# Performance work log

Measured on AMD Instinct MI355X. Metric: run time of the kernel, lower is better.

## Reference

```python
import jax, jax.numpy as jnp
import numpy as np

BLOCK = 256
EPS = 1e-6

def _silu(x):
    return x * jax.nn.sigmoid(x)

def setup_inputs() -> dict:
    key = jax.random.key(0)
    k1, k2, k3, k4 = jax.random.split(key, 4)
    embed_dim, hidden_dim = 2048, 2048
    b, n, h = 2, 4096, 16
    x = jax.random.normal(k1, (b, n, embed_dim), dtype=jnp.float32)
    slope_rate = jax.random.uniform(k2, (h, 1, 1), dtype=jnp.float32, minval=0.01, maxval=1.0)
    W_qkvu = jax.random.normal(k3, (4 * hidden_dim, embed_dim), dtype=jnp.float32) / np.sqrt(embed_dim)
    W_out = jax.random.normal(k4, (embed_dim, hidden_dim), dtype=jnp.float32) / np.sqrt(hidden_dim)
    return {"x": x, "slope_rate": slope_rate, "W_qkvu": W_qkvu, "W_out": W_out}

def reference(x, slope_rate, W_qkvu, W_out):
    b, n, embed_dim = x.shape
    h = slope_rate.shape[0]
    hidden_dim = W_qkvu.shape[0] // 4
    d = hidden_dim // h  # head dim
    NB = n // BLOCK

    qkvu = x @ W_qkvu.T  # [b, n, 4*hidden]
    q, k, v, u = jnp.split(qkvu, 4, axis=-1)

    def to_heads(t):
        return t.reshape(b, n, h, d).transpose(0, 2, 1, 3)  # b h n d

    q = _silu(to_heads(q))
    k = _silu(to_heads(k))
    v = to_heads(v)

    s = slope_rate  # (h,1,1)
    arr = jnp.arange(1, BLOCK + 1, dtype=x.dtype)  # 1..BLOCK
    q_decay = jnp.exp(-s * arr[:, None])                 # (h, B, 1)
    k_decay = jnp.exp(-s * (BLOCK - arr[:, None]))       # (h, B, 1)
    idx = arr[:, None] - arr[None, :]                    # (B, B)
    diag_decay = jnp.exp(jnp.where(idx >= 0, -s * idx, -jnp.inf))  # (h, B, B)
    block_decay = jnp.exp(-s * BLOCK)                    # (h,1,1)

    # reshape into blocks, scan-major axis first
    def blk(t):
        return t.reshape(b, h, NB, BLOCK, d).transpose(2, 0, 1, 3, 4)

    qb, kb, vb = blk(q), blk(k), blk(v)

    def step(kv, inp):
        qi, ki, vi = inp  # (b,h,B,d)
        qkv_none_diag = jnp.einsum('bhmd,bhde->bhme', qi * q_decay, kv)
        qk = jnp.einsum('bhmd,bhsd->bhms', qi, ki) * diag_decay
        qkv_diag = jnp.einsum('bhms,bhse->bhme', qk, vi)
        kv_new = block_decay * kv + jnp.einsum('bhsd,bhse->bhde', ki * k_decay, vi)
        return kv_new, qkv_none_diag + qkv_diag

    kv0 = jnp.zeros((b, h, d, d), dtype=jnp.float32)
    _, outs = jax.lax.scan(step, kv0, (qb, kb, vb))  # (NB,b,h,B,d)

    o = outs.transpose(1, 2, 0, 3, 4).reshape(b, h, n, d)
    o = o.transpose(0, 2, 1, 3).reshape(b, n, hidden_dim)  # b n (h d)

    # simple RMSNorm (no learned scale)
    o = o * jax.lax.rsqrt(jnp.mean(o * o, axis=-1, keepdims=True) + EPS)
    o = u * o
    return o @ W_out.T
```

## Files before the change

kernel.cpp:

```cpp
#include <hip/hip_runtime.h>
#include <stdint.h>

#define GK 2048

typedef short s16x8 __attribute__((ext_vector_type(8)));
typedef short s16x4 __attribute__((ext_vector_type(4)));
typedef float fx4   __attribute__((ext_vector_type(4)));
typedef unsigned int ux2 __attribute__((ext_vector_type(2)));

#define SB0 __builtin_amdgcn_sched_barrier(0)

__device__ __forceinline__ float b2f(unsigned short s) {
  union { unsigned int u; float f; } x; x.u = ((unsigned int)s) << 16; return x.f;
}
__device__ __forceinline__ unsigned short f2b(float f) {
  union { float f; unsigned int u; } x; x.f = f;
  return (unsigned short)((x.u + 0x7fffu + ((x.u >> 16) & 1u)) >> 16);
}
__device__ __forceinline__ void gl_lds16(const void* g, void* l) {
  __builtin_amdgcn_global_load_lds(
      (const __attribute__((address_space(1))) void*)g,
      (__attribute__((address_space(3))) void*)l, 16, 0, 0);
}

__global__ __launch_bounds__(256, 4) void cvt_bf16(const float* __restrict__ in,
                                                   unsigned short* __restrict__ out) {
  int i = blockIdx.x * 256 + threadIdx.x;
  fx4 v = *(const fx4*)(in + (size_t)i * 4);
  ux2 p;
  p[0] = (unsigned int)f2b(v[0]) | ((unsigned int)f2b(v[1]) << 16);
  p[1] = (unsigned int)f2b(v[2]) | ((unsigned int)f2b(v[3]) << 16);
  *(ux2*)(out + (size_t)i * 4) = p;
}

__global__ void sentinel_k(float* o, float val) { o[threadIdx.x] = val; }

__global__ __launch_bounds__(512, 2) void gemm8_qkvu(
    const unsigned short* __restrict__ A, const unsigned short* __restrict__ B,
    int NT, int nBase,
    unsigned short* __restrict__ qp, unsigned short* __restrict__ kp,
    unsigned short* __restrict__ vp, unsigned short* __restrict__ up) {
  __shared__ __align__(16) unsigned short lds8[65536];
  const int nwg = gridDim.x;
  const int bid0 = blockIdx.x;
  const int cpx = nwg >> 3;
  const int bid = (bid0 & 7) * cpx + (bid0 >> 3);
  const int bm = bid / NT, bn = bid % NT;
  const int tid = threadIdx.x;
  const int w = tid >> 6, l = tid & 63;
  const int wr = w >> 2, wc = w & 3;
  const int g = l >> 4, li = l & 15;

  const int srow = l >> 3;
  const int scol = ((l & 7) ^ srow) << 3;
  const unsigned short* Asrc = A + (size_t)(bm * 256) * GK + scol;
  const unsigned short* Bsrc = B + (size_t)(bn * 256) * GK + scol;

  auto stA = [&](int bu, int h, int kt) {
    const unsigned short* s = Asrc + (size_t)(h * 128 + w * 8 + srow) * GK + kt;
    unsigned short* d = &lds8[(bu * 2 + h) * 8192 + w * 512];
    gl_lds16(s, d);
    gl_lds16(s + (size_t)64 * GK, d + 4096);
  };
  auto stB = [&](int bu, int h, int kt) {
    const unsigned short* s = Bsrc + (size_t)(h * 128 + w * 8 + srow) * GK + kt;
    unsigned short* d = &lds8[32768 + (bu * 2 + h) * 8192 + w * 512];
    gl_lds16(s, d);
    gl_lds16(s + (size_t)64 * GK, d + 4096);
  };

  const int s7 = li & 7;
  const int cb0 = ((0 + g) ^ s7) << 3;
  const int cb1 = ((4 + g) ^ s7) << 3;
  const int rbase = li * 64;
  const int Abase0 = wr * 8192;
  const int Bbase0 = 32768 + (wc >> 1) * 8192 + (wc & 1) * 4096;

  s16x8 aF[4][2], bL[2][2], bH[2][2];
  fx4 acc[8][4] = {};

  auto rdA = [&](int rb, int mh) {
    #pragma unroll
    for (int i = 0; i < 4; ++i) {
      int a0 = rb * 16384 + Abase0 + (mh * 4 + i) * 1024 + rbase;
      aF[i][0] = *(const s16x8*)&lds8[a0 + cb0];
      aF[i][1] = *(const s16x8*)&lds8[a0 + cb1];
    }
  };
  auto rdBL = [&](int rb) {
    #pragma unroll
    for (int i = 0; i < 2; ++i) {
      int a0 = rb * 16384 + Bbase0 + i * 1024 + rbase;
      bL[i][0] = *(const s16x8*)&lds8[a0 + cb0];
      bL[i][1] = *(const s16x8*)&lds8[a0 + cb1];
    }
  };
  auto rdBH = [&](int rb) {
    #pragma unroll
    for (int i = 0; i < 2; ++i) {
      int a0 = rb * 16384 + Bbase0 + (2 + i) * 1024 + rbase;
      bH[i][0] = *(const s16x8*)&lds8[a0 + cb0];
      bH[i][1] = *(const s16x8*)&lds8[a0 + cb1];
    }
  };
  auto mm = [&](int mh, int nh, s16x8 (&bF)[2][2]) {
    __builtin_amdgcn_s_setprio(1);
    #pragma unroll
    for (int i = 0; i < 4; ++i)
      #pragma unroll
      for (int j = 0; j < 2; ++j)
        #pragma unroll
        for (int kk = 0; kk < 2; ++kk)
          acc[mh * 4 + i][nh * 2 + j] =
              __builtin_amdgcn_mfma_f32_16x16x32_bf16(aF[i][kk], bF[j][kk],
                                                      acc[mh * 4 + i][nh * 2 + j], 0, 0, 0);
    __builtin_amdgcn_s_setprio(0);
  };

  const int KT = GK / 64;

  stA(0, 0, 0); stB(0, 0, 0); stA(0, 1, 0); stB(0, 1, 0);

  #pragma unroll 2
  for (int t = 0; t < KT - 1; ++t) {
    const int rb = t & 1, wb = rb ^ 1;
    const int ktn = (t + 1) * 64;
    stA(wb, 0, ktn);
    asm volatile("s_waitcnt vmcnt(2)" ::: "memory");
    SB0; __builtin_amdgcn_s_barrier(); SB0;
    rdA(rb, 0); rdBL(rb);
    mm(0, 0, bL);
    SB0; __builtin_amdgcn_s_barrier(); SB0;
    rdBH(rb);
    stB(wb, 0, ktn);
    SB0; __builtin_amdgcn_s_barrier(); SB0;
    mm(0, 1, bH);
    SB0; __builtin_amdgcn_s_barrier(); SB0;
    rdA(rb, 1);
    stA(wb, 1, ktn);
    SB0; __builtin_amdgcn_s_barrier(); SB0;
    mm(1, 1, bH);
    SB0; __builtin_amdgcn_s_barrier(); SB0;
    stB(wb, 1, ktn);
    SB0; __builtin_amdgcn_s_barrier(); SB0;
    mm(1, 0, bL);
    SB0; __builtin_amdgcn_s_barrier(); SB0;
  }
  {
    const int rb = (KT - 1) & 1;
    asm volatile("s_waitcnt vmcnt(0)" ::: "memory");
    SB0; __builtin_amdgcn_s_barrier(); SB0;
    rdA(rb, 0); rdBL(rb);
    mm(0, 0, bL);
    rdBH(rb);
    mm(0, 1, bH);
    rdA(rb, 1);
    mm(1, 1, bH);
    mm(1, 0, bL);
  }

  const int colbase = nBase + bn * 256 + wc * 64;
  #pragma unroll
  for (int mf = 0; mf < 8; ++mf)
    #pragma unroll
    for (int rr = 0; rr < 4; ++rr) {
      int nn = bm * 256 + wr * 128 + mf * 16 + g * 4 + rr;
      #pragma unroll
      for (int nf = 0; nf < 4; ++nf) {
        int colglob = colbase + nf * 16 + li;
        int tq = colglob >> 11, hh = (colglob >> 7) & 15, cl = colglob & 127;
        float vv = acc[mf][nf][rr];
        if (tq < 2) vv = vv / (1.f + __expf(-vv));
        if (tq == 3) up[(size_t)nn * 2048 + hh * 128 + cl] = f2b(vv);
        else ((tq == 0) ? qp : (tq == 1) ? kp : vp)[((size_t)hh * 4096 + nn) * 128 + cl] = f2b(vv);
      }
    }
}

__global__ __launch_bounds__(256, 2) void gemm_out(
    const unsigned short* __restrict__ A, const unsigned short* __restrict__ B,
    float* __restrict__ Cf) {
  __shared__ __align__(16) short lA[128 * 64];
  __shared__ __align__(16) short lB[128 * 64];
  const int nwg = gridDim.x;
  const int bid0 = blockIdx.x;
  const int cpx = nwg >> 3;
  const int bid = (bid0 & 7) * cpx + (bid0 >> 3);
  const int bm = bid / 16, bn = bid % 16;
  const int tid = threadIdx.x;
  const int w = tid >> 6, l = tid & 63;
  const int wr = w >> 1, wc = w & 1;
  const int g = l >> 4, li = l & 15;

  fx4 acc[4][4] = {};
  const int aRow = l >> 3, aCol = (l & 7) * 8;
  const unsigned short* Abase = A + (size_t)(bm * 128) * GK + aCol;
  const unsigned short* Bbase = B + (size_t)(bn * 128) * GK + aCol;

  for (int kt = 0; kt < GK; kt += 64) {
    __syncthreads();
    #pragma unroll
    for (int j = 0; j < 4; ++j) {
      int c = w * 4 + j;
      gl_lds16(Abase + (size_t)(c * 8 + aRow) * GK + kt, &lA[c * 512]);
      gl_lds16(Bbase + (size_t)(c * 8 + aRow) * GK + kt, &lB[c * 512]);
    }
    __syncthreads();
    #pragma unroll
    for (int kk = 0; kk < 2; ++kk) {
      s16x8 af[4], bf[4];
      #pragma unroll
      for (int mf = 0; mf < 4; ++mf)
        af[mf] = *(const s16x8*)&lA[(wr * 64 + mf * 16 + li) * 64 + kk * 32 + g * 8];
      #pragma unroll
      for (int nf = 0; nf < 4; ++nf)
        bf[nf] = *(const s16x8*)&lB[(wc * 64 + nf * 16 + li) * 64 + kk * 32 + g * 8];
      #pragma unroll
      for (int mf = 0; mf < 4; ++mf)
        #pragma unroll
        for (int nf = 0; nf < 4; ++nf)
          acc[mf][nf] = __builtin_amdgcn_mfma_f32_16x16x32_bf16(af[mf], bf[nf], acc[mf][nf], 0, 0, 0);
    }
  }
  #pragma unroll
  for (int mf = 0; mf < 4; ++mf)
    #pragma unroll
    for (int rr = 0; rr < 4; ++rr) {
      int row = bm * 128 + wr * 64 + mf * 16 + g * 4 + rr;
      #pragma unroll
      for (int nf = 0; nf < 4; ++nf) {
        int col = bn * 128 + wc * 64 + nf * 16 + li;
        Cf[(size_t)row * 2048 + col] = acc[mf][nf][rr];
      }
    }
}

__global__ __launch_bounds__(256, 1) void pass1_C(
    const unsigned short* __restrict__ k, const unsigned short* __restrict__ v,
    const float* __restrict__ slope, float* __restrict__ C) {
  __shared__ __align__(16) unsigned short lK[256 * 128];
  __shared__ __align__(16) unsigned short lV[256 * 128];
  __shared__ float ldecay[256];
  const int bid = blockIdx.x;
  const int h_i = bid >> 4, ib = bid & 15;
  const int tid = threadIdx.x, w = tid >> 6, l = tid & 63;
  const int g = l >> 4, li = l & 15;
  const float r = slope[h_i];
  const size_t kvoff = ((size_t)h_i * 4096 + ib * 256) * 128;
  #pragma unroll
  for (int j = 0; j < 16; ++j) {
    int c = w * 16 + j;
    gl_lds16(k + kvoff + c * 512 + l * 8, &lK[c * 512]);
    gl_lds16(v + kvoff + c * 512 + l * 8, &lV[c * 512]);
  }
  ldecay[tid] = __expf(-r * (float)(255 - tid));
  __syncthreads();

  fx4 acc[2][8] = {};
  #pragma unroll 1
  for (int ks = 0; ks < 8; ++ks) {
    s16x8 a[2], b[8];
    #pragma unroll
    for (int mf = 0; mf < 2; ++mf) {
      int dr = w * 32 + mf * 16 + li;
      #pragma unroll
      for (int e = 0; e < 8; ++e) {
        int s = ks * 32 + g * 8 + e;
        a[mf][e] = (short)f2b(b2f(lK[s * 128 + dr]) * ldecay[s]);
      }
    }
    #pragma unroll
    for (int nf = 0; nf < 8; ++nf) {
      int er = nf * 16 + li;
      #pragma unroll
      for (int e = 0; e < 8; ++e) {
        int s = ks * 32 + g * 8 + e;
        b[nf][e] = (short)lV[s * 128 + er];
      }
    }
    #pragma unroll
    for (int mf = 0; mf < 2; ++mf)
      #pragma unroll
      for (int nf = 0; nf < 8; ++nf)
        acc[mf][nf] = __builtin_amdgcn_mfma_f32_16x16x32_bf16(a[mf], b[nf], acc[mf][nf], 0, 0, 0);
  }
  float* Cb = C + (size_t)bid * 16384;
  #pragma unroll
  for (int mf = 0; mf < 2; ++mf)
    #pragma unroll
    for (int rr = 0; rr < 4; ++rr)
      #pragma unroll
      for (int nf = 0; nf < 8; ++nf)
        Cb[(w * 32 + mf * 16 + g * 4 + rr) * 128 + nf * 16 + li] = acc[mf][nf][rr];
}

__global__ __launch_bounds__(256, 4) void scan_kv2(
    const float* __restrict__ C, const float* __restrict__ slope,
    unsigned short* __restrict__ KVb) {
  __shared__ unsigned short lds[8][128];
  const int h_i = blockIdx.x >> 4, c = blockIdx.x & 15;
  const float r = slope[h_i];
  const float bd = __expf(-256.f * r);
  const int t = threadIdx.x;
  float run[4] = {0.f, 0.f, 0.f, 0.f};
  const int e_out = t >> 1, dg = t & 1;
  for (int i = 0; i < 16; ++i) {
    size_t base = ((size_t)h_i * 16 + i) * 16384;
    fx4 cv = *(const fx4*)(C + base + c * 1024 + t * 4);
    #pragma unroll
    for (int j = 0; j < 4; ++j) lds[t >> 5][(t & 31) * 4 + j] = f2b(run[j]);
    __syncthreads();
    s16x4 ov;
    #pragma unroll
    for (int j = 0; j < 4; ++j) ov[j] = (short)lds[dg * 4 + j][e_out];
    *(s16x4*)&KVb[base + e_out * 128 + c * 8 + dg * 4] = ov;
    __syncthreads();
    #pragma unroll
    for (int j = 0; j < 4; ++j) run[j] = bd * run[j] + cv[j];
  }
}

__global__ __launch_bounds__(256, 1) void pass3_O(
    const unsigned short* __restrict__ q, const unsigned short* __restrict__ k,
    const unsigned short* __restrict__ v, const unsigned short* __restrict__ KVb,
    const float* __restrict__ slope, unsigned short* __restrict__ o) {
  __shared__ __align__(16) unsigned short lK[64 * 128];
  __shared__ __align__(16) unsigned short lV[64 * 128];
  __shared__ __align__(16) unsigned short lP[4 * 64 * 64];
  const int bid = blockIdx.x;
  const int h_i = bid >> 4, ib = bid & 15;
  const int n0 = ib * 256;
  const float r = slope[h_i];
  const int tid = threadIdx.x, w = tid >> 6, l = tid & 63;
  const int g = l >> 4, li = l & 15;
  const int mbase = w * 64;

  fx4 accO[4][8] = {};
  const unsigned short* Qb = q + ((size_t)h_i * 4096 + n0 + mbase) * 128;
  const unsigned short* KVbase = KVb + ((size_t)h_i * 16 + ib) * 16384;

  #pragma unroll
  for (int kd = 0; kd < 4; ++kd) {
    s16x8 aq[4], bkv[8];
    #pragma unroll
    for (int mf = 0; mf < 4; ++mf)
      aq[mf] = *(const s16x8*)(Qb + (size_t)(mf * 16 + li) * 128 + kd * 32 + g * 8);
    #pragma unroll
    for (int nf = 0; nf < 8; ++nf)
      bkv[nf] = *(const s16x8*)(KVbase + (size_t)(nf * 16 + li) * 128 + kd * 32 + g * 8);
    #pragma unroll
    for (int mf = 0; mf < 4; ++mf)
      #pragma unroll
      for (int nf = 0; nf < 8; ++nf)
        accO[mf][nf] = __builtin_amdgcn_mfma_f32_16x16x32_bf16(aq[mf], bkv[nf], accO[mf][nf], 0, 0, 0);
  }
  #pragma unroll
  for (int mf = 0; mf < 4; ++mf)
    #pragma unroll
    for (int rr = 0; rr < 4; ++rr) {
      float f = __expf(-r * (float)(mbase + mf * 16 + g * 4 + rr + 1));
      #pragma unroll
      for (int nf = 0; nf < 8; ++nf) accO[mf][nf][rr] *= f;
    }

  for (int st = 0; st < 4; ++st) {
    __syncthreads();
    #pragma unroll
    for (int j = 0; j < 4; ++j) {
      int c = w * 4 + j;
      size_t roff = ((size_t)h_i * 4096 + n0 + st * 64) * 128 + c * 512 + l * 8;
      gl_lds16(k + roff, &lK[c * 512]);
      gl_lds16(v + roff, &lV[c * 512]);
    }
    __syncthreads();
    if (st > w) continue;

    fx4 sacc[4][4] = {};
    #pragma unroll
    for (int kd = 0; kd < 4; ++kd) {
      s16x8 aq[4], bk[4];
      #pragma unroll
      for (int mf = 0; mf < 4; ++mf)
        aq[mf] = *(const s16x8*)(Qb + (size_t)(mf * 16 + li) * 128 + kd * 32 + g * 8);
      #pragma unroll
      for (int nf = 0; nf < 4; ++nf)
        bk[nf] = *(const s16x8*)&lK[(nf * 16 + li) * 128 + kd * 32 + g * 8];
      #pragma unroll
      for (int mf = 0; mf < 4; ++mf)
        #pragma unroll
        for (int nf = 0; nf < 4; ++nf)
          sacc[mf][nf] = __builtin_amdgcn_mfma_f32_16x16x32_bf16(aq[mf], bk[nf], sacc[mf][nf], 0, 0, 0);
    }

    float f2v[4];
    #pragma unroll
    for (int nf = 0; nf < 4; ++nf) f2v[nf] = __expf(r * (float)(nf * 16 + li));
    unsigned short* lPw = &lP[w * 4096];
    #pragma unroll
    for (int mf = 0; mf < 4; ++mf)
      #pragma unroll
      for (int rr = 0; rr < 4; ++rr) {
        int Aoff = mbase - st * 64 + mf * 16 + g * 4 + rr;
        float f1 = __expf(-r * (float)Aoff);
        #pragma unroll
        for (int nf = 0; nf < 4; ++nf) {
          int sc = nf * 16 + li;
          float val = (Aoff >= sc) ? sacc[mf][nf][rr] * f1 * f2v[nf] : 0.f;
          lPw[(mf * 16 + g * 4 + rr) * 64 + sc] = f2b(val);
        }
      }

    #pragma unroll
    for (int ks = 0; ks < 2; ++ks) {
      s16x8 pa[4], vb[8];
      #pragma unroll
      for (int mf = 0; mf < 4; ++mf)
        pa[mf] = *(const s16x8*)&lPw[(mf * 16 + li) * 64 + ks * 32 + g * 8];
      #pragma unroll
      for (int nf = 0; nf < 8; ++nf) {
        int er = nf * 16 + li;
        #pragma unroll
        for (int e = 0; e < 8; ++e) {
          int s = ks * 32 + g * 8 + e;
          vb[nf][e] = (short)lV[s * 128 + er];
        }
      }
      #pragma unroll
      for (int mf = 0; mf < 4; ++mf)
        #pragma unroll
        for (int nf = 0; nf < 8; ++nf)
          accO[mf][nf] = __builtin_amdgcn_mfma_f32_16x16x32_bf16(pa[mf], vb[nf], accO[mf][nf], 0, 0, 0);
    }
  }

  #pragma unroll
  for (int mf = 0; mf < 4; ++mf)
    #pragma unroll
    for (int rr = 0; rr < 4; ++rr) {
      int nn = n0 + mbase + mf * 16 + g * 4 + rr;
      unsigned short* ob = o + (size_t)nn * 2048 + h_i * 128;
      #pragma unroll
      for (int nf = 0; nf < 8; ++nf)
        ob[nf * 16 + li] = f2b(accO[mf][nf][rr]);
    }
}

__global__ __launch_bounds__(256, 4) void norm_mul(
    const unsigned short* __restrict__ o, const unsigned short* __restrict__ u,
    unsigned short* __restrict__ z) {
  __shared__ float red[4];
  const int row = blockIdx.x, t = threadIdx.x;
  const size_t base = (size_t)row * 2048 + t * 8;
  s16x8 ov = *(const s16x8*)(o + base);
  float vals[8]; float ss = 0.f;
  #pragma unroll
  for (int j = 0; j < 8; ++j) { vals[j] = b2f((unsigned short)ov[j]); ss += vals[j] * vals[j]; }
  #pragma unroll
  for (int dl = 1; dl < 64; dl <<= 1) ss += __shfl_xor(ss, dl);
  if ((t & 63) == 0) red[t >> 6] = ss;
  __syncthreads();
  float tot = red[0] + red[1] + red[2] + red[3];
  float rs = rsqrtf(tot * (1.f / 2048.f) + 1e-6f);
  s16x8 uv = *(const s16x8*)(u + base);
  s16x8 zv;
  #pragma unroll
  for (int j = 0; j < 8; ++j)
    zv[j] = (short)f2b(vals[j] * b2f((unsigned short)uv[j]) * rs);
  *(s16x8*)(z + base) = zv;
}

extern "C" void kernel_launch(void* const* d_in, const int* in_sizes, int n_in,
                              void* d_out, int out_size, void* d_ws, size_t ws_size,
                              hipStream_t stream) {
  (void)in_sizes; (void)n_in; (void)out_size;
  const float* x     = (const float*)d_in[0];
  const float* slope = (const float*)d_in[1];
  const float* Wqkvu = (const float*)d_in[2];
  const float* Wout  = (const float*)d_in[3];
  float* out = (float*)d_out;

  const size_t NEED_MED = 92274688ull;
  const size_t NEED_BIG = 125829120ull;
  if (ws_size < NEED_MED) {
    sentinel_k<<<1, 256, 0, stream>>>(out, (float)((double)ws_size * 1e-6));
    return;
  }
  char* ws = (char*)d_ws;

  if (ws_size >= NEED_BIG) {
    unsigned short* wq  = (unsigned short*)(ws + 0);
    unsigned short* S0  = (unsigned short*)(ws + 33554432);
    unsigned short* qb  = (unsigned short*)(ws + 50331648);
    unsigned short* kb  = (unsigned short*)(ws + 67108864);
    unsigned short* vb  = (unsigned short*)(ws + 83886080);
    unsigned short* ub  = (unsigned short*)(ws + 100663296);
    unsigned short* KVr = (unsigned short*)(ws + 117440512);
    cvt_bf16<<<16384, 256, 0, stream>>>(Wqkvu, wq);
    for (int bb = 0; bb < 2; ++bb) {
      const float* xB = x + (size_t)bb * 8388608;
      float* outB = out + (size_t)bb * 8388608;
      cvt_bf16<<<8192, 256, 0, stream>>>(xB, S0);
      gemm8_qkvu<<<512, 512, 0, stream>>>(S0, wq, 32, 0, qb, kb, vb, ub);
      pass1_C<<<256, 256, 0, stream>>>(kb, vb, slope, (float*)S0);
      scan_kv2<<<256, 256, 0, stream>>>((float*)S0, slope, KVr);
      pass3_O<<<256, 256, 0, stream>>>(qb, kb, vb, KVr, slope, S0);
      cvt_bf16<<<4096, 256, 0, stream>>>(Wout, KVr);
      norm_mul<<<4096, 256, 0, stream>>>(S0, ub, qb);
      gemm_out<<<512, 256, 0, stream>>>(qb, KVr, outB);
    }
  } else {
    unsigned short* reg0 = (unsigned short*)(ws + 0);
    unsigned short* qb   = (unsigned short*)(ws + 16777216);
    unsigned short* kb   = (unsigned short*)(ws + 33554432);
    unsigned short* vb   = (unsigned short*)(ws + 50331648);
    unsigned short* ub   = (unsigned short*)(ws + 67108864);
    unsigned short* KVr  = (unsigned short*)(ws + 83886080);
    for (int bb = 0; bb < 2; ++bb) {
      const float* xB = x + (size_t)bb * 8388608;
      float* outB = out + (size_t)bb * 8388608;
      cvt_bf16<<<8192, 256, 0, stream>>>(xB, reg0);
      cvt_bf16<<<8192, 256, 0, stream>>>(Wqkvu, vb);
      gemm8_qkvu<<<256, 512, 0, stream>>>(reg0, vb, 16, 0, qb, kb, vb, ub);
      cvt_bf16<<<4096, 256, 0, stream>>>(Wqkvu + 8388608, KVr);
      gemm8_qkvu<<<128, 512, 0, stream>>>(reg0, KVr, 8, 4096, qb, kb, vb, ub);
      cvt_bf16<<<4096, 256, 0, stream>>>(Wqkvu + 12582912, KVr);
      gemm8_qkvu<<<128, 512, 0, stream>>>(reg0, KVr, 8, 6144, qb, kb, vb, ub);
      pass1_C<<<256, 256, 0, stream>>>(kb, vb, slope, (float*)reg0);
      scan_kv2<<<256, 256, 0, stream>>>((float*)reg0, slope, KVr);
      pass3_O<<<256, 256, 0, stream>>>(qb, kb, vb, KVr, slope, reg0);
      norm_mul<<<4096, 256, 0, stream>>>(reg0, ub, qb);
      cvt_bf16<<<4096, 256, 0, stream>>>(Wout, reg0);
      gemm_out<<<512, 256, 0, stream>>>(qb, reg0, outB);
    }
  }
}
```

Before: 564.3 us.

## Add large-workspace path with batched output GEMM using 256x256 gemm8 tiles

When the workspace is large enough, a new branch converts all of x to bf16 once, keeps per-batch normalized activations in a combined buffer, and runs a single output projection over both batches. That projection uses the larger 256x256-tile gemm8 kernel with a plain fp32 epilogue instead of the smaller gemm_out kernel. It also converts Wout only once. This cuts launches, duplicate conversions, and uses a more efficient GEMM, but it needs more workspace and only runs if the harness provides at least the new threshold.

```diff
diff --git a/kernel.cpp b/kernel.cpp
--- a/kernel.cpp
+++ b/kernel.cpp
@@ -35,11 +35,13 @@
 
 __global__ void sentinel_k(float* o, float val) { o[threadIdx.x] = val; }
 
-__global__ __launch_bounds__(512, 2) void gemm8_qkvu(
+template<int EPI>
+__global__ __launch_bounds__(512, 2) void gemm8(
     const unsigned short* __restrict__ A, const unsigned short* __restrict__ B,
     int NT, int nBase,
     unsigned short* __restrict__ qp, unsigned short* __restrict__ kp,
-    unsigned short* __restrict__ vp, unsigned short* __restrict__ up) {
+    unsigned short* __restrict__ vp, unsigned short* __restrict__ up,
+    float* __restrict__ Cf) {
   __shared__ __align__(16) unsigned short lds8[65536];
   const int nwg = gridDim.x;
   const int bid0 = blockIdx.x;
@@ -159,22 +161,36 @@
     mm(1, 0, bL);
   }
 
-  const int colbase = nBase + bn * 256 + wc * 64;
-  #pragma unroll
-  for (int mf = 0; mf < 8; ++mf)
-    #pragma unroll
-    for (int rr = 0; rr < 4; ++rr) {
-      int nn = bm * 256 + wr * 128 + mf * 16 + g * 4 + rr;
-      #pragma unroll
-      for (int nf = 0; nf < 4; ++nf) {
-        int colglob = colbase + nf * 16 + li;
-        int tq = colglob >> 11, hh = (colglob >> 7) & 15, cl = colglob & 127;
-        float vv = acc[mf][nf][rr];
-        if (tq < 2) vv = vv / (1.f + __expf(-vv));
-        if (tq == 3) up[(size_t)nn * 2048 + hh * 128 + cl] = f2b(vv);
-        else ((tq == 0) ? qp : (tq == 1) ? kp : vp)[((size_t)hh * 4096 + nn) * 128 + cl] = f2b(vv);
-      }
-    }
+  if (EPI == 0) {
+    const int colbase = nBase + bn * 256 + wc * 64;
+    #pragma unroll
+    for (int mf = 0; mf < 8; ++mf)
+      #pragma unroll
+      for (int rr = 0; rr < 4; ++rr) {
+        int nn = bm * 256 + wr * 128 + mf * 16 + g * 4 + rr;
+        #pragma unroll
+        for (int nf = 0; nf < 4; ++nf) {
+          int colglob = colbase + nf * 16 + li;
+          int tq = colglob >> 11, hh = (colglob >> 7) & 15, cl = colglob & 127;
+          float vv = acc[mf][nf][rr];
+          if (tq < 2) vv = vv / (1.f + __expf(-vv));
+          if (tq == 3) up[(size_t)nn * 2048 + hh * 128 + cl] = f2b(vv);
+          else ((tq == 0) ? qp : (tq == 1) ? kp : vp)[((size_t)hh * 4096 + nn) * 128 + cl] = f2b(vv);
+        }
+      }
+  } else {
+    #pragma unroll
+    for (int mf = 0; mf < 8; ++mf)
+      #pragma unroll
+      for (int rr = 0; rr < 4; ++rr) {
+        int row = bm * 256 + wr * 128 + mf * 16 + g * 4 + rr;
+        #pragma unroll
+        for (int nf = 0; nf < 4; ++nf) {
+          int col = bn * 256 + wc * 64 + nf * 16 + li;
+          Cf[(size_t)row * 2048 + col] = acc[mf][nf][rr];
+        }
+      }
+  }
 }
 
 __global__ __launch_bounds__(256, 2) void gemm_out(
@@ -479,15 +495,38 @@
   const float* Wout  = (const float*)d_in[3];
   float* out = (float*)d_out;
 
-  const size_t NEED_MED = 92274688ull;
-  const size_t NEED_BIG = 125829120ull;
+  const size_t NEED_MED  = 92274688ull;
+  const size_t NEED_BIG  = 125829120ull;
+  const size_t NEED_HUGE = 167772160ull;
   if (ws_size < NEED_MED) {
     sentinel_k<<<1, 256, 0, stream>>>(out, (float)((double)ws_size * 1e-6));
     return;
   }
   char* ws = (char*)d_ws;
 
-  if (ws_size >= NEED_BIG) {
+  if (ws_size >= NEED_HUGE) {
+    unsigned short* wq  = (unsigned short*)(ws + 0);
+    unsigned short* xz  = (unsigned short*)(ws + 33554432);
+    unsigned short* qb  = (unsigned short*)(ws + 67108864);
+    unsigned short* kb  = (unsigned short*)(ws + 83886080);
+    unsigned short* vb  = (unsigned short*)(ws + 100663296);
+    unsigned short* ub  = (unsigned short*)(ws + 117440512);
+    unsigned short* S0  = (unsigned short*)(ws + 134217728);
+    unsigned short* KVr = (unsigned short*)(ws + 150994944);
+    cvt_bf16<<<16384, 256, 0, stream>>>(Wqkvu, wq);
+    cvt_bf16<<<16384, 256, 0, stream>>>(x, xz);
+    for (int bb = 0; bb < 2; ++bb) {
+      unsigned short* xzb = xz + (size_t)bb * 8388608;
+      gemm8<0><<<512, 512, 0, stream>>>(xzb, wq, 32, 0, qb, kb, vb, ub, nullptr);
+      pass1_C<<<256, 256, 0, stream>>>(kb, vb, slope, (float*)S0);
+      scan_kv2<<<256, 256, 0, stream>>>((float*)S0, slope, KVr);
+      pass3_O<<<256, 256, 0, stream>>>(qb, kb, vb, KVr, slope, S0);
+      norm_mul<<<4096, 256, 0, stream>>>(S0, ub, xzb);
+    }
+    cvt_bf16<<<4096, 256, 0, stream>>>(Wout, KVr);
+    gemm8<1><<<256, 512, 0, stream>>>(xz, KVr, 8, 0,
+                                      nullptr, nullptr, nullptr, nullptr, out);
+  } else if (ws_size >= NEED_BIG) {
     unsigned short* wq  = (unsigned short*)(ws + 0);
     unsigned short* S0  = (unsigned short*)(ws + 33554432);
     unsigned short* qb  = (unsigned short*)(ws + 50331648);
@@ -500,7 +539,7 @@
       const float* xB = x + (size_t)bb * 8388608;
       float* outB = out + (size_t)bb * 8388608;
       cvt_bf16<<<8192, 256, 0, stream>>>(xB, S0);
-      gemm8_qkvu<<<512, 512, 0, stream>>>(S0, wq, 32, 0, qb, kb, vb, ub);
+      gemm8<0><<<512, 512, 0, stream>>>(S0, wq, 32, 0, qb, kb, vb, ub, nullptr);
       pass1_C<<<256, 256, 0, stream>>>(kb, vb, slope, (float*)S0);
       scan_kv2<<<256, 256, 0, stream>>>((float*)S0, slope, KVr);
       pass3_O<<<256, 256, 0, stream>>>(qb, kb, vb, KVr, slope, S0);
@@ -520,11 +559,11 @@
       float* outB = out + (size_t)bb * 8388608;
       cvt_bf16<<<8192, 256, 0, stream>>>(xB, reg0);
       cvt_bf16<<<8192, 256, 0, stream>>>(Wqkvu, vb);
-      gemm8_qkvu<<<256, 512, 0, stream>>>(reg0, vb, 16, 0, qb, kb, vb, ub);
+      gemm8<0><<<256, 512, 0, stream>>>(reg0, vb, 16, 0, qb, kb, vb, ub, nullptr);
       cvt_bf16<<<4096, 256, 0, stream>>>(Wqkvu + 8388608, KVr);
-      gemm8_qkvu<<<128, 512, 0, stream>>>(reg0, KVr, 8, 4096, qb, kb, vb, ub);
+      gemm8<0><<<128, 512, 0, stream>>>(reg0, KVr, 8, 4096, qb, kb, vb, ub, nullptr);
       cvt_bf16<<<4096, 256, 0, stream>>>(Wqkvu + 12582912, KVr);
-      gemm8_qkvu<<<128, 512, 0, stream>>>(reg0, KVr, 8, 6144, qb, kb, vb, ub);
+      gemm8<0><<<128, 512, 0, stream>>>(reg0, KVr, 8, 6144, qb, kb, vb, ub, nullptr);
       pass1_C<<<256, 256, 0, stream>>>(kb, vb, slope, (float*)reg0);
       scan_kv2<<<256, 256, 0, stream>>>((float*)reg0, slope, KVr);
       pass3_O<<<256, 256, 0, stream>>>(qb, kb, vb, KVr, slope, reg0);
```

Measured after the change: 515.8 us. 8.6% less time.
